# Optimization experiments

Measured on AMD Instinct MI355X. Metric: run time of the kernel, lower is better.

The kernel has to match this reference:

```python
import jax, jax.numpy as jnp
import numpy as np

B, N, E, H, D, F = 2, 4096, 128, 8, 16, 512
EPS = 1e-6


def _rms_norm(x, w):
    xf = x.astype(jnp.float32)
    n = xf * jax.lax.rsqrt(jnp.mean(xf * xf, axis=-1, keepdims=True) + EPS)
    return n.astype(x.dtype) * w


def setup_inputs() -> dict:
    key = jax.random.key(0)
    ks = jax.random.split(key, 12)
    s = 1.0 / np.sqrt(E)
    sf = 1.0 / np.sqrt(F)
    coords = jax.random.uniform(ks[10], (B, N, 2))
    dis = jnp.sqrt(jnp.sum((coords[:, :, None, :] - coords[:, None, :, :]) ** 2, -1))
    dis = dis * (1.0 - jnp.eye(N))  # zero diagonal
    return {
        "input1": jax.random.normal(ks[0], (B, N, E), jnp.float32),
        "dis_matrix": dis.astype(jnp.float32),
        "Wq": jax.random.uniform(ks[1], (E, E), jnp.float32, -s, s),
        "Wk": jax.random.uniform(ks[2], (E, E), jnp.float32, -s, s),
        "Wv": jax.random.uniform(ks[3], (E, E), jnp.float32, -s, s),
        "alpha": jnp.float32(1.0),
        "ln1_w": jnp.ones((E,), jnp.float32),
        "ln2_w": jnp.ones((E,), jnp.float32),
        "Wcomb": jax.random.uniform(ks[4], (E, E), jnp.float32, -s, s),
        "W1": jax.random.uniform(ks[5], (F, E), jnp.float32, -s, s),
        "b1": jax.random.uniform(ks[6], (F,), jnp.float32, -s, s),
        "W2": jax.random.uniform(ks[7], (E, F), jnp.float32, -sf, sf),
        "b2": jax.random.uniform(ks[8], (E,), jnp.float32, -sf, sf),
    }


def _sparse_attention_afm(x, dis_matrix, Wq, Wk, Wv, alpha):
    # project and split heads: [B,N,E] -> [B,H,N,D]
    def heads(w):
        return (x @ w.T).reshape(B, N, H, D).transpose(0, 2, 1, 3)
    q, k, v = heads(Wq), heads(Wk), heads(Wv)
    log2n = jnp.float32(np.log2(N))
    dis_weight = jnp.exp(-alpha * log2n * dis_matrix)  # [B,N,N] (i,j)
    k_weight = jnp.exp(k)  # [B,H,N,D]
    w1 = jnp.einsum('bij,bhik->bhjk', dis_weight, k_weight * v)
    w2 = jnp.einsum('bij,bhik->bhjk', dis_weight, k_weight)
    out = jax.nn.sigmoid(q) * (w1 / w2)  # [B,H,N,D]
    return out.transpose(0, 2, 1, 3).reshape(B, N, E)


def reference(input1, dis_matrix, Wq, Wk, Wv, alpha, ln1_w, ln2_w, Wcomb, W1, b1, W2, b2):
    h = _rms_norm(input1, ln1_w)
    attn = _sparse_attention_afm(h, dis_matrix, Wq, Wk, Wv, alpha)
    out1 = input1 + attn @ Wcomb.T
    h2 = _rms_norm(out1, ln2_w)
    ffn = jax.nn.relu(h2 @ W1.T + b1) @ W2.T + b2
    return out1 + ffn
```

## Files before the change

### kernel.cpp

```cpp
#include <hip/hip_runtime.h>

#define NTOK 4096
#define BNROWS 8192
#define EDIM 128
#define FDIM 512

typedef __attribute__((ext_vector_type(8))) short bf16x8;
typedef __attribute__((ext_vector_type(4))) float f32x4;

__device__ __forceinline__ ushort f2bf(float x) {
    union { float f; unsigned u; } c; c.f = x;
    unsigned r = c.u + 0x7FFF + ((c.u >> 16) & 1);
    return (ushort)(r >> 16);
}

__global__ void prep_k(const float* __restrict__ Wq, const float* __restrict__ Wk,
                       const float* __restrict__ Wv, const float* __restrict__ Wc,
                       const float* __restrict__ W1, const float* __restrict__ W2,
                       ushort* __restrict__ Wbf,
                       const float* __restrict__ input1, const float* __restrict__ ln1w,
                       ushort* __restrict__ h_bf) {
    const int bx = blockIdx.x, t = threadIdx.x;
    if (bx < 768) {
        int i = bx * 256 + t;
        const float* src; int off;
        if (i < 16384)       { src = Wq; off = i; }
        else if (i < 32768)  { src = Wk; off = i - 16384; }
        else if (i < 49152)  { src = Wv; off = i - 32768; }
        else if (i < 65536)  { src = Wc; off = i - 49152; }
        else if (i < 131072) { src = W1; off = i - 65536; }
        else                 { src = W2; off = i - 131072; }
        Wbf[i] = f2bf(src[off]);
    } else {
        int row  = (bx - 768) * 4 + (t >> 6);
        int lane = t & 63;
        float2 v = ((const float2*)(input1 + (size_t)row * EDIM))[lane];
        float ss = v.x * v.x + v.y * v.y;
#pragma unroll
        for (int off = 32; off > 0; off >>= 1) ss += __shfl_down(ss, off, 64);
        ss = __shfl(ss, 0, 64);
        float r = rsqrtf(ss * (1.0f / 128.0f) + 1e-6f);
        float2 wv = ((const float2*)ln1w)[lane];
        ushort2 o; o.x = f2bf(v.x * r * wv.x); o.y = f2bf(v.y * r * wv.y);
        ((ushort2*)(h_bf + (size_t)row * EDIM))[lane] = o;
    }
}

#define EB_SIGQ  0
#define EB_RELUB 1
#define EB_ACC   2

template<int EPIL>
__device__ __forceinline__ void mgemm_body(
    const ushort* __restrict__ A, int lda,
    const ushort* __restrict__ B, int ldb,
    float* __restrict__ outF, ushort* __restrict__ outB, int Nout, int colbase,
    const float* __restrict__ bias, int M0, int nchunks)
{
    __shared__ ushort As[32 * 136];
    __shared__ ushort Bs[128 * 136];
    const int t = threadIdx.x, lane = t & 63, wv = t >> 6;
    const int m15 = lane & 15, kq = (lane >> 4) * 8;
    const int c0w = wv * 32;
    f32x4 acc[2][2] = {};

    const int ar = t >> 3, as0 = (t & 7) * 2;
    const int br = t >> 1, bs0 = (t & 1) * 8;

    for (int c = 0; c < nchunks; ++c) {
        if (c) __syncthreads();
        int kb = c * 128;
#pragma unroll
        for (int j = 0; j < 2; ++j) {
            int seg = as0 + j;
            *(bf16x8*)&As[ar * 136 + seg * 8] =
                *(const bf16x8*)&A[(size_t)(M0 + ar) * lda + kb + seg * 8];
        }
#pragma unroll
        for (int j = 0; j < 8; ++j) {
            int seg = bs0 + j;
            *(bf16x8*)&Bs[br * 136 + seg * 8] =
                *(const bf16x8*)&B[(size_t)br * ldb + kb + seg * 8];
        }
        __syncthreads();
#pragma unroll
        for (int kc = 0; kc < 4; ++kc) {
            int ko = kc * 32 + kq;
            bf16x8 a0 = *(const bf16x8*)&As[m15 * 136 + ko];
            bf16x8 a1 = *(const bf16x8*)&As[(16 + m15) * 136 + ko];
            bf16x8 b0 = *(const bf16x8*)&Bs[(c0w + m15) * 136 + ko];
            bf16x8 b1 = *(const bf16x8*)&Bs[(c0w + 16 + m15) * 136 + ko];
            acc[0][0] = __builtin_amdgcn_mfma_f32_16x16x32_bf16(a0, b0, acc[0][0], 0, 0, 0);
            acc[0][1] = __builtin_amdgcn_mfma_f32_16x16x32_bf16(a0, b1, acc[0][1], 0, 0, 0);
            acc[1][0] = __builtin_amdgcn_mfma_f32_16x16x32_bf16(a1, b0, acc[1][0], 0, 0, 0);
            acc[1][1] = __builtin_amdgcn_mfma_f32_16x16x32_bf16(a1, b1, acc[1][1], 0, 0, 0);
        }
    }
#pragma unroll
    for (int mi = 0; mi < 2; ++mi)
#pragma unroll
        for (int ni = 0; ni < 2; ++ni)
#pragma unroll
            for (int r = 0; r < 4; ++r) {
                int row = M0 + mi * 16 + (lane >> 4) * 4 + r;
                int lc  = c0w + ni * 16 + m15;
                size_t off = (size_t)row * Nout + colbase + lc;
                float vv = acc[mi][ni][r];
                if (EPIL == EB_SIGQ)  outF[off] = 1.0f / (1.0f + __expf(-vv));
                if (EPIL == EB_RELUB) outB[off] = f2bf(fmaxf(vv + bias[lc], 0.0f));
                if (EPIL == EB_ACC)   outF[off] += vv;
            }
}

__launch_bounds__(256, 3)
__global__ void q_sig_k(const ushort* __restrict__ h, const ushort* __restrict__ Wbf,
                        float* __restrict__ sigq) {
    mgemm_body<EB_SIGQ>(h, 128, Wbf, 128, sigq, nullptr, 128, 0, nullptr,
                        blockIdx.x * 32, 1);
}

__launch_bounds__(256, 3)
__global__ void ffn1_k(const ushort* __restrict__ h2, const ushort* __restrict__ Wbf,
                       const float* __restrict__ b1, ushort* __restrict__ mid) {
    int N0 = blockIdx.y * 128;
    mgemm_body<EB_RELUB>(h2, 128, Wbf + 65536 + N0 * 128, 128, nullptr, mid, 512, N0,
                         b1 + N0, blockIdx.x * 32, 1);
}

__launch_bounds__(256, 3)
__global__ void ffn2_k(const ushort* __restrict__ mid, const ushort* __restrict__ Wbf,
                       float* __restrict__ outp) {
    mgemm_body<EB_ACC>(mid, 512, Wbf + 131072, 512, outp, nullptr, 128, 0, nullptr,
                       blockIdx.x * 32, 4);
}

__launch_bounds__(256, 3)
__global__ void kv_mt_k(const ushort* __restrict__ h, const ushort* __restrict__ Wbf,
                        ushort* __restrict__ Mt) {
    __shared__ ushort As[32 * 136];
    __shared__ ushort Bs[2][64 * 136];
    const int t = threadIdx.x, lane = t & 63, wv = t >> 6;
    const int m15 = lane & 15, quad = lane >> 4, kq = quad * 8;
    const int M0 = blockIdx.x * 32;
    const int e0 = blockIdx.y * 64;

    const int ar = t >> 3, as0 = (t & 7) * 2;
#pragma unroll
    for (int j = 0; j < 2; ++j) {
        int seg = as0 + j;
        *(bf16x8*)&As[ar * 136 + seg * 8] =
            *(const bf16x8*)&h[(size_t)(M0 + ar) * 128 + seg * 8];
    }
    const int bm = t >> 7;
    const int br = (t & 127) >> 1, bs0 = (t & 1) * 8;
    const ushort* W = Wbf + 16384 + bm * 16384;
#pragma unroll
    for (int j = 0; j < 8; ++j) {
        int seg = bs0 + j;
        *(bf16x8*)&Bs[bm][br * 136 + seg * 8] =
            *(const bf16x8*)&W[(size_t)(e0 + br) * 128 + seg * 8];
    }
    __syncthreads();

    f32x4 acck[2] = {}, accv[2] = {};
    const int cw = wv * 16;
#pragma unroll
    for (int kc = 0; kc < 4; ++kc) {
        int ko = kc * 32 + kq;
        bf16x8 a0 = *(const bf16x8*)&As[m15 * 136 + ko];
        bf16x8 a1 = *(const bf16x8*)&As[(16 + m15) * 136 + ko];
        bf16x8 bk = *(const bf16x8*)&Bs[0][(cw + m15) * 136 + ko];
        bf16x8 bv = *(const bf16x8*)&Bs[1][(cw + m15) * 136 + ko];
        acck[0] = __builtin_amdgcn_mfma_f32_16x16x32_bf16(a0, bk, acck[0], 0, 0, 0);
        acck[1] = __builtin_amdgcn_mfma_f32_16x16x32_bf16(a1, bk, acck[1], 0, 0, 0);
        accv[0] = __builtin_amdgcn_mfma_f32_16x16x32_bf16(a0, bv, accv[0], 0, 0, 0);
        accv[1] = __builtin_amdgcn_mfma_f32_16x16x32_bf16(a1, bv, accv[1], 0, 0, 0);
    }
    const int b  = M0 >> 12;
    const int i0 = M0 & (NTOK - 1);
    const int e  = e0 + cw + m15;
    ushort* mt0 = Mt + ((size_t)b * 256 + e) * NTOK;
    ushort* mt1 = Mt + ((size_t)b * 256 + 128 + e) * NTOK;
#pragma unroll
    for (int mi = 0; mi < 2; ++mi) {
        int ib = i0 + mi * 16 + quad * 4;
        ushort4 pv, pk;
        float kw0 = __expf(acck[mi][0]); pv.x = f2bf(kw0 * accv[mi][0]); pk.x = f2bf(kw0);
        float kw1 = __expf(acck[mi][1]); pv.y = f2bf(kw1 * accv[mi][1]); pk.y = f2bf(kw1);
        float kw2 = __expf(acck[mi][2]); pv.z = f2bf(kw2 * accv[mi][2]); pk.z = f2bf(kw2);
        float kw3 = __expf(acck[mi][3]); pv.w = f2bf(kw3 * accv[mi][3]); pk.w = f2bf(kw3);
        *(ushort4*)&mt0[ib] = pv;
        *(ushort4*)&mt1[ib] = pk;
    }
}

__launch_bounds__(256, 2)
__global__ void big_gemm_k(const float* __restrict__ dis, const float* __restrict__ alphap,
                           const ushort* __restrict__ Mt,
                           float* __restrict__ P0, float* __restrict__ P1) {
    __shared__ ushort As[32 * 72];
    __shared__ ushort Bs[256 * 72];
    const int t = threadIdx.x, lane = t & 63, wv = t >> 6;
    const int m15 = lane & 15, quad = lane >> 4, kq = quad * 8;
    const int j0 = blockIdx.x * 32;
    const int b  = blockIdx.y;
    const int s  = blockIdx.z;
    const float coef = -alphap[0] * 12.0f;
    const float* disb = dis + (size_t)b * NTOK * NTOK;
    const ushort* Mtb = Mt + (size_t)b * 256 * NTOK;
    float* outp = ((s == 0) ? P0 : P1) + (size_t)b * NTOK * 256;

    f32x4 acc[2][4] = {};
    const int aj = t >> 3, ak = (t & 7) * 8;
    const int brow = t >> 3, bseg = (t & 7) * 8;
    const int k0 = s * (NTOK / 2);

    float4 fa0, fa1;
    bf16x8 pb[8];
    {
        const float* ap = disb + (size_t)(j0 + aj) * NTOK + k0 + ak;
        fa0 = *(const float4*)ap; fa1 = *(const float4*)(ap + 4);
#pragma unroll
        for (int p = 0; p < 8; ++p)
            pb[p] = *(const bf16x8*)&Mtb[(size_t)(p * 32 + brow) * NTOK + k0 + bseg];
    }

    for (int it = 0; it < 32; ++it) {
        bf16x8 a8;
        a8[0] = (short)f2bf(__expf(coef * fa0.x));
        a8[1] = (short)f2bf(__expf(coef * fa0.y));
        a8[2] = (short)f2bf(__expf(coef * fa0.z));
        a8[3] = (short)f2bf(__expf(coef * fa0.w));
        a8[4] = (short)f2bf(__expf(coef * fa1.x));
        a8[5] = (short)f2bf(__expf(coef * fa1.y));
        a8[6] = (short)f2bf(__expf(coef * fa1.z));
        a8[7] = (short)f2bf(__expf(coef * fa1.w));
        *(bf16x8*)&As[aj * 72 + ak] = a8;
#pragma unroll
        for (int p = 0; p < 8; ++p)
            *(bf16x8*)&Bs[(p * 32 + brow) * 72 + bseg] = pb[p];
        __syncthreads();
        if (it < 31) {
            int kn = k0 + (it + 1) * 64;
            const float* ap = disb + (size_t)(j0 + aj) * NTOK + kn + ak;
            fa0 = *(const float4*)ap; fa1 = *(const float4*)(ap + 4);
#pragma unroll
            for (int p = 0; p < 8; ++p)
                pb[p] = *(const bf16x8*)&Mtb[(size_t)(p * 32 + brow) * NTOK + kn + bseg];
        }
#pragma unroll
        for (int kh = 0; kh < 2; ++kh) {
            int ko = kh * 32 + kq;
            bf16x8 a0 = *(const bf16x8*)&As[m15 * 72 + ko];
            bf16x8 a1 = *(const bf16x8*)&As[(16 + m15) * 72 + ko];
#pragma unroll
            for (int ni = 0; ni < 4; ++ni) {
                bf16x8 bv = *(const bf16x8*)&Bs[(wv * 64 + ni * 16 + m15) * 72 + ko];
                acc[0][ni] = __builtin_amdgcn_mfma_f32_16x16x32_bf16(a0, bv, acc[0][ni], 0, 0, 0);
                acc[1][ni] = __builtin_amdgcn_mfma_f32_16x16x32_bf16(a1, bv, acc[1][ni], 0, 0, 0);
            }
        }
        __syncthreads();
    }
#pragma unroll
    for (int mi = 0; mi < 2; ++mi)
#pragma unroll
        for (int ni = 0; ni < 4; ++ni)
#pragma unroll
            for (int r = 0; r < 4; ++r) {
                int j = j0 + mi * 16 + quad * 4 + r;
                int c = wv * 64 + ni * 16 + m15;
                outp[(size_t)j * 256 + c] = acc[mi][ni][r];
            }
}

__launch_bounds__(256, 2)
__global__ void wcomb_rms2_k(const float* __restrict__ sigq,
                             const float* __restrict__ P0, const float* __restrict__ P1,
                             const ushort* __restrict__ Wbf,
                             const float* __restrict__ input1, const float* __restrict__ b2,
                             const float* __restrict__ ln2w,
                             float* __restrict__ outD, ushort* __restrict__ h2) {
    __shared__ ushort As[32 * 136];
    __shared__ ushort Bs[128 * 136];
    __shared__ float  O[32][132];
    const int t = threadIdx.x, lane = t & 63, wv = t >> 6;
    const int m15 = lane & 15, quad = lane >> 4, kq = quad * 8;
    const int M0 = blockIdx.x * 32;

    {
        const int ar = t >> 3, e0 = (t & 7) * 16;
        const int g = M0 + ar;
        const float4* sg = (const float4*)(sigq + (size_t)g * 128 + e0);
        const float4* p0a = (const float4*)(P0 + (size_t)g * 256 + e0);
        const float4* p1a = (const float4*)(P1 + (size_t)g * 256 + e0);
        const float4* p0b = (const float4*)(P0 + (size_t)g * 256 + 128 + e0);
        const float4* p1b = (const float4*)(P1 + (size_t)g * 256 + 128 + e0);
#pragma unroll
        for (int i = 0; i < 4; ++i) {
            float4 s = sg[i];
            float4 u0 = p0a[i], u1 = p1a[i], d0 = p0b[i], d1 = p1b[i];
            ushort4 a;
            a.x = f2bf(s.x * (u0.x + u1.x) / (d0.x + d1.x));
            a.y = f2bf(s.y * (u0.y + u1.y) / (d0.y + d1.y));
            a.z = f2bf(s.z * (u0.z + u1.z) / (d0.z + d1.z));
            a.w = f2bf(s.w * (u0.w + u1.w) / (d0.w + d1.w));
            *(ushort4*)&As[ar * 136 + e0 + i * 4] = a;
        }
    }
    {
        const int br = t >> 1, bs0 = (t & 1) * 8;
        const ushort* W = Wbf + 49152;
#pragma unroll
        for (int j = 0; j < 8; ++j) {
            int seg = bs0 + j;
            *(bf16x8*)&Bs[br * 136 + seg * 8] =
                *(const bf16x8*)&W[(size_t)br * 128 + seg * 8];
        }
    }
    __syncthreads();

    f32x4 acc[2][2] = {};
    const int c0w = wv * 32;
#pragma unroll
    for (int kc = 0; kc < 4; ++kc) {
        int ko = kc * 32 + kq;
        bf16x8 a0 = *(const bf16x8*)&As[m15 * 136 + ko];
        bf16x8 a1 = *(const bf16x8*)&As[(16 + m15) * 136 + ko];
        bf16x8 b0 = *(const bf16x8*)&Bs[(c0w + m15) * 136 + ko];
        bf16x8 b1 = *(const bf16x8*)&Bs[(c0w + 16 + m15) * 136 + ko];
        acc[0][0] = __builtin_amdgcn_mfma_f32_16x16x32_bf16(a0, b0, acc[0][0], 0, 0, 0);
        acc[0][1] = __builtin_amdgcn_mfma_f32_16x16x32_bf16(a0, b1, acc[0][1], 0, 0, 0);
        acc[1][0] = __builtin_amdgcn_mfma_f32_16x16x32_bf16(a1, b0, acc[1][0], 0, 0, 0);
        acc[1][1] = __builtin_amdgcn_mfma_f32_16x16x32_bf16(a1, b1, acc[1][1], 0, 0, 0);
    }
#pragma unroll
    for (int mi = 0; mi < 2; ++mi)
#pragma unroll
        for (int ni = 0; ni < 2; ++ni)
#pragma unroll
            for (int r = 0; r < 4; ++r) {
                int rl = mi * 16 + quad * 4 + r;
                int col = c0w + ni * 16 + m15;
                size_t off = (size_t)(M0 + rl) * 128 + col;
                float v = acc[mi][ni][r] + input1[off];
                O[rl][col] = v;
                outD[off] = v + b2[col];
            }
    __syncthreads();
    {
        const int row = t >> 3, seg = t & 7;
        float4 x[4];
        float ss = 0.f;
#pragma unroll
        for (int i = 0; i < 4; ++i) {
            x[i] = *(const float4*)&O[row][seg * 16 + i * 4];
            ss += x[i].x * x[i].x + x[i].y * x[i].y + x[i].z * x[i].z + x[i].w * x[i].w;
        }
        ss += __shfl_down(ss, 4, 8);
        ss += __shfl_down(ss, 2, 8);
        ss += __shfl_down(ss, 1, 8);
        ss = __shfl(ss, 0, 8);
        float rr = rsqrtf(ss * (1.0f / 128.0f) + 1e-6f);
        ushort* hp = h2 + (size_t)(M0 + row) * 128 + seg * 16;
#pragma unroll
        for (int i = 0; i < 4; ++i) {
            float4 wv4 = *(const float4*)&ln2w[seg * 16 + i * 4];
            ushort4 o;
            o.x = f2bf(x[i].x * rr * wv4.x);
            o.y = f2bf(x[i].y * rr * wv4.y);
            o.z = f2bf(x[i].z * rr * wv4.z);
            o.w = f2bf(x[i].w * rr * wv4.w);
            *(ushort4*)&hp[i * 4] = o;
        }
    }
}

extern "C" void kernel_launch(void* const* d_in, const int* in_sizes, int n_in,
                              void* d_out, int out_size, void* d_ws, size_t ws_size,
                              hipStream_t stream) {
    const float* input1 = (const float*)d_in[0];
    const float* dis    = (const float*)d_in[1];
    const float* Wq     = (const float*)d_in[2];
    const float* Wk     = (const float*)d_in[3];
    const float* Wv     = (const float*)d_in[4];
    const float* alpha  = (const float*)d_in[5];
    const float* ln1    = (const float*)d_in[6];
    const float* ln2    = (const float*)d_in[7];
    const float* Wcomb  = (const float*)d_in[8];
    const float* W1     = (const float*)d_in[9];
    const float* b1     = (const float*)d_in[10];
    const float* W2     = (const float*)d_in[11];
    const float* b2     = (const float*)d_in[12];
    float* out = (float*)d_out;

    char* w8 = (char*)d_ws;
    ushort* Wbf  = (ushort*)(w8);
    ushort* h_bf = (ushort*)(w8 + (1u << 20));
    float*  sigq = (float*)(w8 + (4u << 20));
    ushort* Mt   = (ushort*)(w8 + (8u << 20));
    float*  P0   = (float*)(w8 + (12u << 20));
    float*  P1   = (float*)(w8 + (20u << 20));
    ushort* h2   = (ushort*)(w8 + (1u << 20));
    ushort* mid  = (ushort*)(w8 + (12u << 20));

    prep_k<<<dim3(2816), 256, 0, stream>>>(Wq, Wk, Wv, Wcomb, W1, W2, Wbf,
                                           input1, ln1, h_bf);
    q_sig_k<<<dim3(256), 256, 0, stream>>>(h_bf, Wbf, sigq);
    kv_mt_k<<<dim3(256, 2), 256, 0, stream>>>(h_bf, Wbf, Mt);
    big_gemm_k<<<dim3(128, 2, 2), 256, 0, stream>>>(dis, alpha, Mt, P0, P1);
    wcomb_rms2_k<<<dim3(256), 256, 0, stream>>>(sigq, P0, P1, Wbf, input1, b2,
                                                ln2, out, h2);
    ffn1_k<<<dim3(256, 4), 256, 0, stream>>>(h2, Wbf, b1, mid);
    ffn2_k<<<dim3(256), 256, 0, stream>>>(mid, Wbf, out);
}
```

Measured before the change: 270.1 us.

## Fuse pipeline into three kernels: QKV prep, retiled big GEMM, fused tail FFN

Merges the seven-kernel pipeline into three. The first kernel does RMS norm, weight conversion and the Q/K/V projections. The big distance-weighted GEMM is retiled to 512 threads with 64-row tiles and register double-buffering. A single tail kernel then does Wcomb, the second RMS norm and both FFN GEMMs, keeping intermediates in shared memory. The aim is to cut launch overhead and global round trips for h, h2 and mid, at the cost of heavy LDS use and low occupancy in the tail kernel.

```diff
diff --git a/kernel.cpp b/kernel.cpp
--- a/kernel.cpp
+++ b/kernel.cpp
@@ -1,9 +1,7 @@
 #include <hip/hip_runtime.h>
 
 #define NTOK 4096
-#define BNROWS 8192
 #define EDIM 128
-#define FDIM 512
 
 typedef __attribute__((ext_vector_type(8))) short bf16x8;
 typedef __attribute__((ext_vector_type(4))) float f32x4;
@@ -14,314 +12,28 @@
     return (ushort)(r >> 16);
 }
 
-__global__ void prep_k(const float* __restrict__ Wq, const float* __restrict__ Wk,
-                       const float* __restrict__ Wv, const float* __restrict__ Wc,
-                       const float* __restrict__ W1, const float* __restrict__ W2,
-                       ushort* __restrict__ Wbf,
-                       const float* __restrict__ input1, const float* __restrict__ ln1w,
-                       ushort* __restrict__ h_bf) {
-    const int bx = blockIdx.x, t = threadIdx.x;
-    if (bx < 768) {
-        int i = bx * 256 + t;
-        const float* src; int off;
-        if (i < 16384)       { src = Wq; off = i; }
-        else if (i < 32768)  { src = Wk; off = i - 16384; }
-        else if (i < 49152)  { src = Wv; off = i - 32768; }
-        else if (i < 65536)  { src = Wc; off = i - 49152; }
-        else if (i < 131072) { src = W1; off = i - 65536; }
-        else                 { src = W2; off = i - 131072; }
-        Wbf[i] = f2bf(src[off]);
-    } else {
-        int row  = (bx - 768) * 4 + (t >> 6);
-        int lane = t & 63;
-        float2 v = ((const float2*)(input1 + (size_t)row * EDIM))[lane];
-        float ss = v.x * v.x + v.y * v.y;
-#pragma unroll
-        for (int off = 32; off > 0; off >>= 1) ss += __shfl_down(ss, off, 64);
-        ss = __shfl(ss, 0, 64);
-        float r = rsqrtf(ss * (1.0f / 128.0f) + 1e-6f);
-        float2 wv = ((const float2*)ln1w)[lane];
-        ushort2 o; o.x = f2bf(v.x * r * wv.x); o.y = f2bf(v.y * r * wv.y);
-        ((ushort2*)(h_bf + (size_t)row * EDIM))[lane] = o;
-    }
-}
-
-#define EB_SIGQ  0
-#define EB_RELUB 1
-#define EB_ACC   2
-
-template<int EPIL>
-__device__ __forceinline__ void mgemm_body(
-    const ushort* __restrict__ A, int lda,
-    const ushort* __restrict__ B, int ldb,
-    float* __restrict__ outF, ushort* __restrict__ outB, int Nout, int colbase,
-    const float* __restrict__ bias, int M0, int nchunks)
-{
-    __shared__ ushort As[32 * 136];
-    __shared__ ushort Bs[128 * 136];
-    const int t = threadIdx.x, lane = t & 63, wv = t >> 6;
-    const int m15 = lane & 15, kq = (lane >> 4) * 8;
-    const int c0w = wv * 32;
-    f32x4 acc[2][2] = {};
-
-    const int ar = t >> 3, as0 = (t & 7) * 2;
-    const int br = t >> 1, bs0 = (t & 1) * 8;
-
-    for (int c = 0; c < nchunks; ++c) {
-        if (c) __syncthreads();
-        int kb = c * 128;
-#pragma unroll
-        for (int j = 0; j < 2; ++j) {
-            int seg = as0 + j;
-            *(bf16x8*)&As[ar * 136 + seg * 8] =
-                *(const bf16x8*)&A[(size_t)(M0 + ar) * lda + kb + seg * 8];
-        }
-#pragma unroll
-        for (int j = 0; j < 8; ++j) {
-            int seg = bs0 + j;
-            *(bf16x8*)&Bs[br * 136 + seg * 8] =
-                *(const bf16x8*)&B[(size_t)br * ldb + kb + seg * 8];
-        }
-        __syncthreads();
-#pragma unroll
-        for (int kc = 0; kc < 4; ++kc) {
-            int ko = kc * 32 + kq;
-            bf16x8 a0 = *(const bf16x8*)&As[m15 * 136 + ko];
-            bf16x8 a1 = *(const bf16x8*)&As[(16 + m15) * 136 + ko];
-            bf16x8 b0 = *(const bf16x8*)&Bs[(c0w + m15) * 136 + ko];
-            bf16x8 b1 = *(const bf16x8*)&Bs[(c0w + 16 + m15) * 136 + ko];
-            acc[0][0] = __builtin_amdgcn_mfma_f32_16x16x32_bf16(a0, b0, acc[0][0], 0, 0, 0);
-            acc[0][1] = __builtin_amdgcn_mfma_f32_16x16x32_bf16(a0, b1, acc[0][1], 0, 0, 0);
-            acc[1][0] = __builtin_amdgcn_mfma_f32_16x16x32_bf16(a1, b0, acc[1][0], 0, 0, 0);
-            acc[1][1] = __builtin_amdgcn_mfma_f32_16x16x32_bf16(a1, b1, acc[1][1], 0, 0, 0);
-        }
-    }
-#pragma unroll
-    for (int mi = 0; mi < 2; ++mi)
-#pragma unroll
-        for (int ni = 0; ni < 2; ++ni)
-#pragma unroll
-            for (int r = 0; r < 4; ++r) {
-                int row = M0 + mi * 16 + (lane >> 4) * 4 + r;
-                int lc  = c0w + ni * 16 + m15;
-                size_t off = (size_t)row * Nout + colbase + lc;
-                float vv = acc[mi][ni][r];
-                if (EPIL == EB_SIGQ)  outF[off] = 1.0f / (1.0f + __expf(-vv));
-                if (EPIL == EB_RELUB) outB[off] = f2bf(fmaxf(vv + bias[lc], 0.0f));
-                if (EPIL == EB_ACC)   outF[off] += vv;
-            }
-}
-
-__launch_bounds__(256, 3)
-__global__ void q_sig_k(const ushort* __restrict__ h, const ushort* __restrict__ Wbf,
-                        float* __restrict__ sigq) {
-    mgemm_body<EB_SIGQ>(h, 128, Wbf, 128, sigq, nullptr, 128, 0, nullptr,
-                        blockIdx.x * 32, 1);
-}
-
-__launch_bounds__(256, 3)
-__global__ void ffn1_k(const ushort* __restrict__ h2, const ushort* __restrict__ Wbf,
-                       const float* __restrict__ b1, ushort* __restrict__ mid) {
-    int N0 = blockIdx.y * 128;
-    mgemm_body<EB_RELUB>(h2, 128, Wbf + 65536 + N0 * 128, 128, nullptr, mid, 512, N0,
-                         b1 + N0, blockIdx.x * 32, 1);
-}
-
-__launch_bounds__(256, 3)
-__global__ void ffn2_k(const ushort* __restrict__ mid, const ushort* __restrict__ Wbf,
-                       float* __restrict__ outp) {
-    mgemm_body<EB_ACC>(mid, 512, Wbf + 131072, 512, outp, nullptr, 128, 0, nullptr,
-                       blockIdx.x * 32, 4);
-}
-
-__launch_bounds__(256, 3)
-__global__ void kv_mt_k(const ushort* __restrict__ h, const ushort* __restrict__ Wbf,
-                        ushort* __restrict__ Mt) {
-    __shared__ ushort As[32 * 136];
-    __shared__ ushort Bs[2][64 * 136];
-    const int t = threadIdx.x, lane = t & 63, wv = t >> 6;
-    const int m15 = lane & 15, quad = lane >> 4, kq = quad * 8;
-    const int M0 = blockIdx.x * 32;
-    const int e0 = blockIdx.y * 64;
-
-    const int ar = t >> 3, as0 = (t & 7) * 2;
-#pragma unroll
-    for (int j = 0; j < 2; ++j) {
-        int seg = as0 + j;
-        *(bf16x8*)&As[ar * 136 + seg * 8] =
-            *(const bf16x8*)&h[(size_t)(M0 + ar) * 128 + seg * 8];
-    }
-    const int bm = t >> 7;
-    const int br = (t & 127) >> 1, bs0 = (t & 1) * 8;
-    const ushort* W = Wbf + 16384 + bm * 16384;
+__device__ __forceinline__ void stage_w(const float* __restrict__ W, ushort* Bs) {
+    const int t = threadIdx.x;
+    const int br = t >> 1, h = (t & 1) * 64;
+    const float* src = W + (size_t)br * 128 + h;
+    ushort* dst = Bs + br * 136 + h;
 #pragma unroll
     for (int j = 0; j < 8; ++j) {
-        int seg = bs0 + j;
-        *(bf16x8*)&Bs[bm][br * 136 + seg * 8] =
-            *(const bf16x8*)&W[(size_t)(e0 + br) * 128 + seg * 8];
-    }
-    __syncthreads();
-
-    f32x4 acck[2] = {}, accv[2] = {};
-    const int cw = wv * 16;
-#pragma unroll
-    for (int kc = 0; kc < 4; ++kc) {
-        int ko = kc * 32 + kq;
-        bf16x8 a0 = *(const bf16x8*)&As[m15 * 136 + ko];
-        bf16x8 a1 = *(const bf16x8*)&As[(16 + m15) * 136 + ko];
-        bf16x8 bk = *(const bf16x8*)&Bs[0][(cw + m15) * 136 + ko];
-        bf16x8 bv = *(const bf16x8*)&Bs[1][(cw + m15) * 136 + ko];
-        acck[0] = __builtin_amdgcn_mfma_f32_16x16x32_bf16(a0, bk, acck[0], 0, 0, 0);
-        acck[1] = __builtin_amdgcn_mfma_f32_16x16x32_bf16(a1, bk, acck[1], 0, 0, 0);
-        accv[0] = __builtin_amdgcn_mfma_f32_16x16x32_bf16(a0, bv, accv[0], 0, 0, 0);
-        accv[1] = __builtin_amdgcn_mfma_f32_16x16x32_bf16(a1, bv, accv[1], 0, 0, 0);
-    }
-    const int b  = M0 >> 12;
-    const int i0 = M0 & (NTOK - 1);
-    const int e  = e0 + cw + m15;
-    ushort* mt0 = Mt + ((size_t)b * 256 + e) * NTOK;
-    ushort* mt1 = Mt + ((size_t)b * 256 + 128 + e) * NTOK;
-#pragma unroll
-    for (int mi = 0; mi < 2; ++mi) {
-        int ib = i0 + mi * 16 + quad * 4;
-        ushort4 pv, pk;
-        float kw0 = __expf(acck[mi][0]); pv.x = f2bf(kw0 * accv[mi][0]); pk.x = f2bf(kw0);
-        float kw1 = __expf(acck[mi][1]); pv.y = f2bf(kw1 * accv[mi][1]); pk.y = f2bf(kw1);
-        float kw2 = __expf(acck[mi][2]); pv.z = f2bf(kw2 * accv[mi][2]); pk.z = f2bf(kw2);
-        float kw3 = __expf(acck[mi][3]); pv.w = f2bf(kw3 * accv[mi][3]); pk.w = f2bf(kw3);
-        *(ushort4*)&mt0[ib] = pv;
-        *(ushort4*)&mt1[ib] = pk;
-    }
-}
-
-__launch_bounds__(256, 2)
-__global__ void big_gemm_k(const float* __restrict__ dis, const float* __restrict__ alphap,
-                           const ushort* __restrict__ Mt,
-                           float* __restrict__ P0, float* __restrict__ P1) {
-    __shared__ ushort As[32 * 72];
-    __shared__ ushort Bs[256 * 72];
-    const int t = threadIdx.x, lane = t & 63, wv = t >> 6;
-    const int m15 = lane & 15, quad = lane >> 4, kq = quad * 8;
-    const int j0 = blockIdx.x * 32;
-    const int b  = blockIdx.y;
-    const int s  = blockIdx.z;
-    const float coef = -alphap[0] * 12.0f;
-    const float* disb = dis + (size_t)b * NTOK * NTOK;
-    const ushort* Mtb = Mt + (size_t)b * 256 * NTOK;
-    float* outp = ((s == 0) ? P0 : P1) + (size_t)b * NTOK * 256;
-
-    f32x4 acc[2][4] = {};
-    const int aj = t >> 3, ak = (t & 7) * 8;
-    const int brow = t >> 3, bseg = (t & 7) * 8;
-    const int k0 = s * (NTOK / 2);
-
-    float4 fa0, fa1;
-    bf16x8 pb[8];
-    {
-        const float* ap = disb + (size_t)(j0 + aj) * NTOK + k0 + ak;
-        fa0 = *(const float4*)ap; fa1 = *(const float4*)(ap + 4);
-#pragma unroll
-        for (int p = 0; p < 8; ++p)
-            pb[p] = *(const bf16x8*)&Mtb[(size_t)(p * 32 + brow) * NTOK + k0 + bseg];
-    }
-
-    for (int it = 0; it < 32; ++it) {
-        bf16x8 a8;
-        a8[0] = (short)f2bf(__expf(coef * fa0.x));
-        a8[1] = (short)f2bf(__expf(coef * fa0.y));
-        a8[2] = (short)f2bf(__expf(coef * fa0.z));
-        a8[3] = (short)f2bf(__expf(coef * fa0.w));
-        a8[4] = (short)f2bf(__expf(coef * fa1.x));
-        a8[5] = (short)f2bf(__expf(coef * fa1.y));
-        a8[6] = (short)f2bf(__expf(coef * fa1.z));
-        a8[7] = (short)f2bf(__expf(coef * fa1.w));
-        *(bf16x8*)&As[aj * 72 + ak] = a8;
-#pragma unroll
-        for (int p = 0; p < 8; ++p)
-            *(bf16x8*)&Bs[(p * 32 + brow) * 72 + bseg] = pb[p];
-        __syncthreads();
-        if (it < 31) {
-            int kn = k0 + (it + 1) * 64;
-            const float* ap = disb + (size_t)(j0 + aj) * NTOK + kn + ak;
-            fa0 = *(const float4*)ap; fa1 = *(const float4*)(ap + 4);
-#pragma unroll
-            for (int p = 0; p < 8; ++p)
-                pb[p] = *(const bf16x8*)&Mtb[(size_t)(p * 32 + brow) * NTOK + kn + bseg];
-        }
-#pragma unroll
-        for (int kh = 0; kh < 2; ++kh) {
-            int ko = kh * 32 + kq;
-            bf16x8 a0 = *(const bf16x8*)&As[m15 * 72 + ko];
-            bf16x8 a1 = *(const bf16x8*)&As[(16 + m15) * 72 + ko];
-#pragma unroll
-            for (int ni = 0; ni < 4; ++ni) {
-                bf16x8 bv = *(const bf16x8*)&Bs[(wv * 64 + ni * 16 + m15) * 72 + ko];
-                acc[0][ni] = __builtin_amdgcn_mfma_f32_16x16x32_bf16(a0, bv, acc[0][ni], 0, 0, 0);
-                acc[1][ni] = __builtin_amdgcn_mfma_f32_16x16x32_bf16(a1, bv, acc[1][ni], 0, 0, 0);
-            }
-        }
-        __syncthreads();
-    }
-#pragma unroll
-    for (int mi = 0; mi < 2; ++mi)
-#pragma unroll
-        for (int ni = 0; ni < 4; ++ni)
-#pragma unroll
-            for (int r = 0; r < 4; ++r) {
-                int j = j0 + mi * 16 + quad * 4 + r;
-                int c = wv * 64 + ni * 16 + m15;
-                outp[(size_t)j * 256 + c] = acc[mi][ni][r];
-            }
-}
-
-__launch_bounds__(256, 2)
-__global__ void wcomb_rms2_k(const float* __restrict__ sigq,
-                             const float* __restrict__ P0, const float* __restrict__ P1,
-                             const ushort* __restrict__ Wbf,
-                             const float* __restrict__ input1, const float* __restrict__ b2,
-                             const float* __restrict__ ln2w,
-                             float* __restrict__ outD, ushort* __restrict__ h2) {
-    __shared__ ushort As[32 * 136];
-    __shared__ ushort Bs[128 * 136];
-    __shared__ float  O[32][132];
-    const int t = threadIdx.x, lane = t & 63, wv = t >> 6;
-    const int m15 = lane & 15, quad = lane >> 4, kq = quad * 8;
-    const int M0 = blockIdx.x * 32;
-
-    {
-        const int ar = t >> 3, e0 = (t & 7) * 16;
-        const int g = M0 + ar;
-        const float4* sg = (const float4*)(sigq + (size_t)g * 128 + e0);
-        const float4* p0a = (const float4*)(P0 + (size_t)g * 256 + e0);
-        const float4* p1a = (const float4*)(P1 + (size_t)g * 256 + e0);
-        const float4* p0b = (const float4*)(P0 + (size_t)g * 256 + 128 + e0);
-        const float4* p1b = (const float4*)(P1 + (size_t)g * 256 + 128 + e0);
-#pragma unroll
-        for (int i = 0; i < 4; ++i) {
-            float4 s = sg[i];
-            float4 u0 = p0a[i], u1 = p1a[i], d0 = p0b[i], d1 = p1b[i];
-            ushort4 a;
-            a.x = f2bf(s.x * (u0.x + u1.x) / (d0.x + d1.x));
-            a.y = f2bf(s.y * (u0.y + u1.y) / (d0.y + d1.y));
-            a.z = f2bf(s.z * (u0.z + u1.z) / (d0.z + d1.z));
-            a.w = f2bf(s.w * (u0.w + u1.w) / (d0.w + d1.w));
-            *(ushort4*)&As[ar * 136 + e0 + i * 4] = a;
-        }
-    }
-    {
-        const int br = t >> 1, bs0 = (t & 1) * 8;
-        const ushort* W = Wbf + 49152;
-#pragma unroll
-        for (int j = 0; j < 8; ++j) {
-            int seg = bs0 + j;
-            *(bf16x8*)&Bs[br * 136 + seg * 8] =
-                *(const bf16x8*)&W[(size_t)br * 128 + seg * 8];
-        }
-    }
-    __syncthreads();
-
-    f32x4 acc[2][2] = {};
-    const int c0w = wv * 32;
+        float4 u = *(const float4*)(src + j * 8);
+        float4 v = *(const float4*)(src + j * 8 + 4);
+        bf16x8 o;
+        o[0] = (short)f2bf(u.x); o[1] = (short)f2bf(u.y);
+        o[2] = (short)f2bf(u.z); o[3] = (short)f2bf(u.w);
+        o[4] = (short)f2bf(v.x); o[5] = (short)f2bf(v.y);
+        o[6] = (short)f2bf(v.z); o[7] = (short)f2bf(v.w);
+        *(bf16x8*)(dst + j * 8) = o;
+    }
+}
+
+__device__ __forceinline__ void gemm128(const ushort* __restrict__ As,
+                                        const ushort* __restrict__ Bs,
+                                        f32x4 (&acc)[2][2], int lane, int wv) {
+    const int m15 = lane & 15, kq = (lane >> 4) * 8, c0w = wv * 32;
 #pragma unroll
     for (int kc = 0; kc < 4; ++kc) {
         int ko = kc * 32 + kq;
@@ -334,27 +46,41 @@
         acc[1][0] = __builtin_amdgcn_mfma_f32_16x16x32_bf16(a1, b0, acc[1][0], 0, 0, 0);
         acc[1][1] = __builtin_amdgcn_mfma_f32_16x16x32_bf16(a1, b1, acc[1][1], 0, 0, 0);
     }
-#pragma unroll
-    for (int mi = 0; mi < 2; ++mi)
-#pragma unroll
-        for (int ni = 0; ni < 2; ++ni)
-#pragma unroll
-            for (int r = 0; r < 4; ++r) {
-                int rl = mi * 16 + quad * 4 + r;
-                int col = c0w + ni * 16 + m15;
-                size_t off = (size_t)(M0 + rl) * 128 + col;
-                float v = acc[mi][ni][r] + input1[off];
-                O[rl][col] = v;
-                outD[off] = v + b2[col];
-            }
-    __syncthreads();
+}
+
+__launch_bounds__(256, 2)
+__global__ void qkv_k(const float* __restrict__ input1, const float* __restrict__ ln1w,
+                      const float* __restrict__ Wq, const float* __restrict__ Wk,
+                      const float* __restrict__ Wv,
+                      const float* __restrict__ Wc, const float* __restrict__ W1,
+                      const float* __restrict__ W2, ushort* __restrict__ Wbf,
+                      float* __restrict__ sigq, ushort* __restrict__ Mt) {
+    const int bx = blockIdx.x;
+    if (bx >= 256) {
+        int g = ((bx - 256) * 256 + threadIdx.x) * 4;
+        const float* src; ushort* dst;
+        if (g < 16384)      { src = Wc + g;           dst = Wbf + 49152 + g; }
+        else if (g < 81920) { src = W1 + (g - 16384); dst = Wbf + 65536 + (g - 16384); }
+        else                { src = W2 + (g - 81920); dst = Wbf + 131072 + (g - 81920); }
+        float4 u = *(const float4*)src;
+        ushort4 o; o.x = f2bf(u.x); o.y = f2bf(u.y); o.z = f2bf(u.z); o.w = f2bf(u.w);
+        *(ushort4*)dst = o;
+        return;
+    }
+    __shared__ ushort As[32 * 136];
+    __shared__ ushort Bs0[128 * 136];
+    __shared__ ushort Bs1[128 * 136];
+    const int t = threadIdx.x, lane = t & 63, wv = t >> 6;
+    const int m15 = lane & 15, quad = lane >> 4, c0w = wv * 32;
+    const int M0 = bx * 32;
+
     {
         const int row = t >> 3, seg = t & 7;
-        float4 x[4];
-        float ss = 0.f;
-#pragma unroll
-        for (int i = 0; i < 4; ++i) {
-            x[i] = *(const float4*)&O[row][seg * 16 + i * 4];
+        const float* xp = input1 + (size_t)(M0 + row) * 128 + seg * 16;
+        float4 x[4]; float ss = 0.f;
+#pragma unroll
+        for (int i = 0; i < 4; ++i) {
+            x[i] = *(const float4*)(xp + i * 4);
             ss += x[i].x * x[i].x + x[i].y * x[i].y + x[i].z * x[i].z + x[i].w * x[i].w;
         }
         ss += __shfl_down(ss, 4, 8);
@@ -362,18 +88,273 @@
         ss += __shfl_down(ss, 1, 8);
         ss = __shfl(ss, 0, 8);
         float rr = rsqrtf(ss * (1.0f / 128.0f) + 1e-6f);
-        ushort* hp = h2 + (size_t)(M0 + row) * 128 + seg * 16;
-#pragma unroll
-        for (int i = 0; i < 4; ++i) {
-            float4 wv4 = *(const float4*)&ln2w[seg * 16 + i * 4];
+#pragma unroll
+        for (int i = 0; i < 4; ++i) {
+            float4 w4 = *(const float4*)&ln1w[seg * 16 + i * 4];
             ushort4 o;
-            o.x = f2bf(x[i].x * rr * wv4.x);
-            o.y = f2bf(x[i].y * rr * wv4.y);
-            o.z = f2bf(x[i].z * rr * wv4.z);
-            o.w = f2bf(x[i].w * rr * wv4.w);
-            *(ushort4*)&hp[i * 4] = o;
-        }
-    }
+            o.x = f2bf(x[i].x * rr * w4.x);
+            o.y = f2bf(x[i].y * rr * w4.y);
+            o.z = f2bf(x[i].z * rr * w4.z);
+            o.w = f2bf(x[i].w * rr * w4.w);
+            *(ushort4*)&As[row * 136 + seg * 16 + i * 4] = o;
+        }
+    }
+    stage_w(Wq, Bs0);
+    __syncthreads();
+    {
+        f32x4 acc[2][2] = {};
+        gemm128(As, Bs0, acc, lane, wv);
+        stage_w(Wk, Bs1);
+#pragma unroll
+        for (int mi = 0; mi < 2; ++mi)
+#pragma unroll
+            for (int ni = 0; ni < 2; ++ni)
+#pragma unroll
+                for (int r = 0; r < 4; ++r) {
+                    int row = M0 + mi * 16 + quad * 4 + r;
+                    int lc  = c0w + ni * 16 + m15;
+                    sigq[(size_t)row * 128 + lc] = 1.0f / (1.0f + __expf(-acc[mi][ni][r]));
+                }
+    }
+    __syncthreads();
+    f32x4 acck[2][2] = {};
+    gemm128(As, Bs1, acck, lane, wv);
+    stage_w(Wv, Bs0);
+    __syncthreads();
+    f32x4 accv[2][2] = {};
+    gemm128(As, Bs0, accv, lane, wv);
+    const int b = M0 >> 12, i0 = M0 & (NTOK - 1);
+#pragma unroll
+    for (int mi = 0; mi < 2; ++mi)
+#pragma unroll
+        for (int ni = 0; ni < 2; ++ni) {
+            int e = c0w + ni * 16 + m15;
+            ushort* mt0 = Mt + ((size_t)b * 256 + e) * NTOK;
+            ushort* mt1 = mt0 + (size_t)128 * NTOK;
+            int ib = i0 + mi * 16 + quad * 4;
+            ushort4 pv, pk;
+            float kw0 = __expf(acck[mi][ni][0]); pv.x = f2bf(kw0 * accv[mi][ni][0]); pk.x = f2bf(kw0);
+            float kw1 = __expf(acck[mi][ni][1]); pv.y = f2bf(kw1 * accv[mi][ni][1]); pk.y = f2bf(kw1);
+            float kw2 = __expf(acck[mi][ni][2]); pv.z = f2bf(kw2 * accv[mi][ni][2]); pk.z = f2bf(kw2);
+            float kw3 = __expf(acck[mi][ni][3]); pv.w = f2bf(kw3 * accv[mi][ni][3]); pk.w = f2bf(kw3);
+            *(ushort4*)&mt0[ib] = pv;
+            *(ushort4*)&mt1[ib] = pk;
+        }
+}
+
+__launch_bounds__(512, 2)
+__global__ void big_gemm_k(const float* __restrict__ dis, const float* __restrict__ alphap,
+                           const ushort* __restrict__ Mt,
+                           float* __restrict__ P0, float* __restrict__ P1) {
+    __shared__ ushort As[64 * 72];
+    const int P = blockIdx.x;
+    const int q = (P & 7) >> 1;
+    const int b = q & 1, s = q >> 1;
+    const int j0 = (((P >> 3) << 1) | (P & 1)) * 64;
+    const int t = threadIdx.x, lane = t & 63, wv = t >> 6;
+    const int m15 = lane & 15, quad = lane >> 4, kq = quad * 8;
+    const float coef = -alphap[0] * 12.0f;
+    const float* disb = dis + (size_t)b * NTOK * NTOK;
+    const ushort* Mtb = Mt + (size_t)b * 256 * NTOK;
+    float* outp = ((s == 0) ? P0 : P1) + (size_t)b * NTOK * 256;
+    const int k0 = s * (NTOK / 2);
+
+    const int aj = t >> 3, ak = (t & 7) * 8;
+    const float* arow = disb + (size_t)(j0 + aj) * NTOK;
+    const int c0 = wv * 32;
+    const ushort* Bp = Mtb + (size_t)(c0 + m15) * NTOK + kq;
+
+    f32x4 acc[4][2] = {};
+    float4 fA0, fA1, fB0, fB1;
+    bf16x8 pb[2][2], pbn[2][2];
+    fA0 = *(const float4*)(arow + k0 + ak);
+    fA1 = *(const float4*)(arow + k0 + ak + 4);
+    fB0 = *(const float4*)(arow + k0 + 64 + ak);
+    fB1 = *(const float4*)(arow + k0 + 64 + ak + 4);
+#pragma unroll
+    for (int kh = 0; kh < 2; ++kh)
+#pragma unroll
+        for (int ni = 0; ni < 2; ++ni)
+            pb[kh][ni] = *(const bf16x8*)&Bp[(size_t)(ni * 16) * NTOK + k0 + kh * 32];
+
+#define BIG_ITER(FA0, FA1, PBC, PBN, IT) do {                                   \
+    bf16x8 a8;                                                                  \
+    a8[0] = (short)f2bf(__expf(coef * FA0.x));                                  \
+    a8[1] = (short)f2bf(__expf(coef * FA0.y));                                  \
+    a8[2] = (short)f2bf(__expf(coef * FA0.z));                                  \
+    a8[3] = (short)f2bf(__expf(coef * FA0.w));                                  \
+    a8[4] = (short)f2bf(__expf(coef * FA1.x));                                  \
+    a8[5] = (short)f2bf(__expf(coef * FA1.y));                                  \
+    a8[6] = (short)f2bf(__expf(coef * FA1.z));                                  \
+    a8[7] = (short)f2bf(__expf(coef * FA1.w));                                  \
+    *(bf16x8*)&As[aj * 72 + ak] = a8;                                           \
+    __syncthreads();                                                            \
+    {   int itA = (IT) + 2; int ka = (itA < 32) ? k0 + itA * 64 : k0;           \
+        FA0 = *(const float4*)(arow + ka + ak);                                 \
+        FA1 = *(const float4*)(arow + ka + ak + 4);                             \
+        int itB = (IT) + 1; int kb_ = (itB < 32) ? k0 + itB * 64 : k0;          \
+        _Pragma("unroll") for (int kh = 0; kh < 2; ++kh)                        \
+        _Pragma("unroll") for (int ni = 0; ni < 2; ++ni)                        \
+            PBN[kh][ni] = *(const bf16x8*)&Bp[(size_t)(ni * 16) * NTOK + kb_ + kh * 32]; } \
+    _Pragma("unroll") for (int kh = 0; kh < 2; ++kh) {                          \
+        bf16x8 av0 = *(const bf16x8*)&As[(m15) * 72 + kh * 32 + kq];            \
+        bf16x8 av1 = *(const bf16x8*)&As[(16 + m15) * 72 + kh * 32 + kq];       \
+        bf16x8 av2 = *(const bf16x8*)&As[(32 + m15) * 72 + kh * 32 + kq];       \
+        bf16x8 av3 = *(const bf16x8*)&As[(48 + m15) * 72 + kh * 32 + kq];       \
+        acc[0][0] = __builtin_amdgcn_mfma_f32_16x16x32_bf16(av0, PBC[kh][0], acc[0][0], 0, 0, 0); \
+        acc[0][1] = __builtin_amdgcn_mfma_f32_16x16x32_bf16(av0, PBC[kh][1], acc[0][1], 0, 0, 0); \
+        acc[1][0] = __builtin_amdgcn_mfma_f32_16x16x32_bf16(av1, PBC[kh][0], acc[1][0], 0, 0, 0); \
+        acc[1][1] = __builtin_amdgcn_mfma_f32_16x16x32_bf16(av1, PBC[kh][1], acc[1][1], 0, 0, 0); \
+        acc[2][0] = __builtin_amdgcn_mfma_f32_16x16x32_bf16(av2, PBC[kh][0], acc[2][0], 0, 0, 0); \
+        acc[2][1] = __builtin_amdgcn_mfma_f32_16x16x32_bf16(av2, PBC[kh][1], acc[2][1], 0, 0, 0); \
+        acc[3][0] = __builtin_amdgcn_mfma_f32_16x16x32_bf16(av3, PBC[kh][0], acc[3][0], 0, 0, 0); \
+        acc[3][1] = __builtin_amdgcn_mfma_f32_16x16x32_bf16(av3, PBC[kh][1], acc[3][1], 0, 0, 0); \
+    }                                                                           \
+    __syncthreads();                                                            \
+} while (0)
+
+    for (int it2 = 0; it2 < 16; ++it2) {
+        BIG_ITER(fA0, fA1, pb, pbn, it2 * 2);
+        BIG_ITER(fB0, fB1, pbn, pb, it2 * 2 + 1);
+    }
+#undef BIG_ITER
+
+#pragma unroll
+    for (int mi = 0; mi < 4; ++mi)
+#pragma unroll
+        for (int ni = 0; ni < 2; ++ni)
+#pragma unroll
+            for (int r = 0; r < 4; ++r) {
+                int j = j0 + mi * 16 + quad * 4 + r;
+                int c = c0 + ni * 16 + m15;
+                outp[(size_t)j * 256 + c] = acc[mi][ni][r];
+            }
+}
+
+__launch_bounds__(256, 1)
+__global__ void tail_k(const float* __restrict__ sigq,
+                       const float* __restrict__ P0, const float* __restrict__ P1,
+                       const ushort* __restrict__ Wbf,
+                       const float* __restrict__ input1, const float* __restrict__ b1,
+                       const float* __restrict__ b2, const float* __restrict__ ln2w,
+                       float* __restrict__ out) {
+    __shared__ ushort As[32 * 136];
+    __shared__ ushort As2[32 * 136];
+    __shared__ ushort Bs[128 * 136];
+    __shared__ ushort Bs2[128 * 136];
+    __shared__ float  O[32][132];
+    const int t = threadIdx.x, lane = t & 63, wv = t >> 6;
+    const int m15 = lane & 15, quad = lane >> 4, c0w = wv * 32;
+    const int M0 = blockIdx.x * 32;
+
+    {
+        const int ar = t >> 3, e0 = (t & 7) * 16;
+        const int g = M0 + ar;
+        const float4* sg  = (const float4*)(sigq + (size_t)g * 128 + e0);
+        const float4* p0a = (const float4*)(P0 + (size_t)g * 256 + e0);
+        const float4* p1a = (const float4*)(P1 + (size_t)g * 256 + e0);
+        const float4* p0b = (const float4*)(P0 + (size_t)g * 256 + 128 + e0);
+        const float4* p1b = (const float4*)(P1 + (size_t)g * 256 + 128 + e0);
+#pragma unroll
+        for (int i = 0; i < 4; ++i) {
+            float4 s = sg[i];
+            float4 u0 = p0a[i], u1 = p1a[i], d0 = p0b[i], d1 = p1b[i];
+            ushort4 a;
+            a.x = f2bf(s.x * (u0.x + u1.x) / (d0.x + d1.x));
+            a.y = f2bf(s.y * (u0.y + u1.y) / (d0.y + d1.y));
+            a.z = f2bf(s.z * (u0.z + u1.z) / (d0.z + d1.z));
+            a.w = f2bf(s.w * (u0.w + u1.w) / (d0.w + d1.w));
+            *(ushort4*)&As[ar * 136 + e0 + i * 4] = a;
+        }
+    }
+    {
+        const int br = t >> 1, bs0 = (t & 1) * 8;
+        const ushort* W = Wbf + 49152;
+#pragma unroll
+        for (int j = 0; j < 8; ++j) {
+            int seg = bs0 + j;
+            *(bf16x8*)&Bs[br * 136 + seg * 8] = *(const bf16x8*)&W[(size_t)br * 128 + seg * 8];
+        }
+    }
+    __syncthreads();
+    f32x4 acc[2][2] = {};
+    gemm128(As, Bs, acc, lane, wv);
+#pragma unroll
+    for (int mi = 0; mi < 2; ++mi)
+#pragma unroll
+        for (int ni = 0; ni < 2; ++ni)
+#pragma unroll
+            for (int r = 0; r < 4; ++r) {
+                int rl  = mi * 16 + quad * 4 + r;
+                int col = c0w + ni * 16 + m15;
+                O[rl][col] = acc[mi][ni][r] + input1[(size_t)(M0 + rl) * 128 + col];
+            }
+    __syncthreads();
+    {
+        const int row = t >> 3, seg = t & 7;
+        float4 x[4]; float ss = 0.f;
+#pragma unroll
+        for (int i = 0; i < 4; ++i) {
+            x[i] = *(const float4*)&O[row][seg * 16 + i * 4];
+            ss += x[i].x * x[i].x + x[i].y * x[i].y + x[i].z * x[i].z + x[i].w * x[i].w;
+        }
+        ss += __shfl_down(ss, 4, 8);
+        ss += __shfl_down(ss, 2, 8);
+        ss += __shfl_down(ss, 1, 8);
+        ss = __shfl(ss, 0, 8);
+        float rr = rsqrtf(ss * (1.0f / 128.0f) + 1e-6f);
+#pragma unroll
+        for (int i = 0; i < 4; ++i) {
+            float4 w4 = *(const float4*)&ln2w[seg * 16 + i * 4];
+            ushort4 o;
+            o.x = f2bf(x[i].x * rr * w4.x);
+            o.y = f2bf(x[i].y * rr * w4.y);
+            o.z = f2bf(x[i].z * rr * w4.z);
+            o.w = f2bf(x[i].w * rr * w4.w);
+            *(ushort4*)&As[row * 136 + seg * 16 + i * 4] = o;
+        }
+    }
+    f32x4 aout[2][2] = {};
+    for (int f0 = 0; f0 < 4; ++f0) {
+        __syncthreads();
+        {
+            const int br = t >> 1, h = (t & 1) * 64;
+            const ushort* w1 = Wbf + 65536 + (size_t)(f0 * 128 + br) * 128 + h;
+            const ushort* w2 = Wbf + 131072 + (size_t)br * 512 + f0 * 128 + h;
+            ushort* d1 = Bs + br * 136 + h;
+            ushort* d2 = Bs2 + br * 136 + h;
+#pragma unroll
+            for (int j = 0; j < 8; ++j) {
+                *(bf16x8*)(d1 + j * 8) = *(const bf16x8*)(w1 + j * 8);
+                *(bf16x8*)(d2 + j * 8) = *(const bf16x8*)(w2 + j * 8);
+            }
+        }
+        __syncthreads();
+        f32x4 am[2][2] = {};
+        gemm128(As, Bs, am, lane, wv);
+#pragma unroll
+        for (int mi = 0; mi < 2; ++mi)
+#pragma unroll
+            for (int ni = 0; ni < 2; ++ni)
+#pragma unroll
+                for (int r = 0; r < 4; ++r) {
+                    int rl  = mi * 16 + quad * 4 + r;
+                    int col = c0w + ni * 16 + m15;
+                    As2[rl * 136 + col] = f2bf(fmaxf(am[mi][ni][r] + b1[f0 * 128 + col], 0.0f));
+                }
+        __syncthreads();
+        gemm128(As2, Bs2, aout, lane, wv);
+    }
+#pragma unroll
+    for (int mi = 0; mi < 2; ++mi)
+#pragma unroll
+        for (int ni = 0; ni < 2; ++ni)
+#pragma unroll
+            for (int r = 0; r < 4; ++r) {
+                int rl  = mi * 16 + quad * 4 + r;
+                int col = c0w + ni * 16 + m15;
+                out[(size_t)(M0 + rl) * 128 + col] = (O[rl][col] + b2[col]) + aout[mi][ni][r];
+            }
 }
 
 extern "C" void kernel_launch(void* const* d_in, const int* in_sizes, int n_in,
@@ -396,21 +377,14 @@
 
     char* w8 = (char*)d_ws;
     ushort* Wbf  = (ushort*)(w8);
-    ushort* h_bf = (ushort*)(w8 + (1u << 20));
     float*  sigq = (float*)(w8 + (4u << 20));
     ushort* Mt   = (ushort*)(w8 + (8u << 20));
     float*  P0   = (float*)(w8 + (12u << 20));
     float*  P1   = (float*)(w8 + (20u << 20));
-    ushort* h2   = (ushort*)(w8 + (1u << 20));
-    ushort* mid  = (ushort*)(w8 + (12u << 20));
-
-    prep_k<<<dim3(2816), 256, 0, stream>>>(Wq, Wk, Wv, Wcomb, W1, W2, Wbf,
-                                           input1, ln1, h_bf);
-    q_sig_k<<<dim3(256), 256, 0, stream>>>(h_bf, Wbf, sigq);
-    kv_mt_k<<<dim3(256, 2), 256, 0, stream>>>(h_bf, Wbf, Mt);
-    big_gemm_k<<<dim3(128, 2, 2), 256, 0, stream>>>(dis, alpha, Mt, P0, P1);
-    wcomb_rms2_k<<<dim3(256), 256, 0, stream>>>(sigq, P0, P1, Wbf, input1, b2,
-                                                ln2, out, h2);
-    ffn1_k<<<dim3(256, 4), 256, 0, stream>>>(h2, Wbf, b1, mid);
-    ffn2_k<<<dim3(256), 256, 0, stream>>>(mid, Wbf, out);
-}
+
+    qkv_k<<<dim3(400), 256, 0, stream>>>(input1, ln1, Wq, Wk, Wv,
+                                         Wcomb, W1, W2, Wbf, sigq, Mt);
+    big_gemm_k<<<dim3(256), 512, 0, stream>>>(dis, alpha, Mt, P0, P1);
+    tail_k<<<dim3(256), 256, 0, stream>>>(sigq, P0, P1, Wbf, input1, b1, b2,
+                                          ln2, out);
+}
```

Result: no change. 264.9 us (-1.9%).
